# Performance work log

Hardware: AMD Instinct MI355X
Metric: run time of the kernel (lower is better)

## Reference

```python
import jax, jax.numpy as jnp
import numpy as np
import math

C = 128
LAM = 0.25
MARGIN = 0.3
TAU = math.log(C)
B = 8192


def lambertw(z, iters=10):
    """Principal-branch Lambert W via Halley iterations (valid for z >= -1/e)."""
    e = jnp.exp(1.0)
    # series init near the branch point z = -1/e, log init for z >= 0
    p = jnp.sqrt(jnp.maximum(2.0 * (e * z + 1.0), 0.0))
    w_near = -1.0 + p - p * p / 3.0 + (11.0 / 72.0) * p ** 3
    w = jnp.where(z < 0.0, w_near, jnp.log1p(jnp.maximum(z, 0.0)))
    for _ in range(iters):
        ew = jnp.exp(w)
        f = w * ew - z
        wp1 = w + 1.0
        w = w - f / (ew * wp1 - (w + 2.0) * f / (2.0 * wp1))
    return w


def triplet_loss(x, targets):
    # pairwise euclidean distances [B, B]
    sq = jnp.sum(x * x, axis=1)
    dist = sq[:, None] + sq[None, :] - 2.0 * (x @ x.T)
    dist = jnp.sqrt(jnp.maximum(dist, 1e-12))
    pos = targets[:, None] == targets[None, :]
    # hardest positive / hardest negative per anchor
    dist_ap = jnp.max(jnp.where(pos, dist, -jnp.inf), axis=1)
    dist_an = jnp.min(jnp.where(pos, jnp.inf, dist), axis=1)
    # MarginRankingLoss(margin)(dist_an, dist_ap, y=1), mean reduction
    return jnp.mean(jnp.maximum(dist_ap - dist_an + MARGIN, 0.0))


def cross_entropy(logits, targets):
    logp = jax.nn.log_softmax(logits, axis=-1)
    return -jnp.mean(jnp.take_along_axis(logp, targets[:, None], axis=1)[:, 0])


def setup_inputs() -> dict:
    key = jax.random.key(0)
    k1, k2 = jax.random.split(key)
    logits = jax.random.normal(k1, (B, C), dtype=jnp.float32)
    targets = jax.random.randint(k2, (B,), 0, C, dtype=jnp.int64)
    return {"logits": logits, "targets": targets}


def reference(logits, targets):
    # l_i is detached in the original (and sigma goes through numpy -> no grad)
    l_i = jax.lax.stop_gradient(triplet_loss(logits, targets))
    y = 0.5 * jnp.maximum(-2.0 / jnp.exp(1.0), (l_i - TAU) / LAM)
    sigma = jax.lax.stop_gradient(jnp.exp(-lambertw(y)))
    ce = cross_entropy(logits, targets)
    loss = (ce - TAU) * sigma + LAM * jnp.log(sigma) ** 2
    return jnp.sum(loss) / B
```

## Files before the change

kernel.cpp:

```cpp
#include <hip/hip_runtime.h>
#include <math.h>

#define NB 8192
#define NC 128
#define NJS 8
#define JPT 8

typedef float v4f __attribute__((ext_vector_type(4)));
typedef int   v8i __attribute__((ext_vector_type(8)));

__global__ __launch_bounds__(256) void k_prep(const float* __restrict__ x,
                                              const int* __restrict__ tgt,
                                              unsigned* __restrict__ xq,
                                              float* __restrict__ sq,
                                              float* __restrict__ ce,
                                              float* __restrict__ sums,
                                              unsigned* __restrict__ cnt) {
    int row = blockIdx.x * 8 + (threadIdx.x >> 5);
    int l = threadIdx.x & 31;
    float4 v = ((const float4*)(x + row * NC))[l];
    unsigned p = __builtin_amdgcn_cvt_pk_fp8_f32(v.x, v.y, 0, false);
    p = __builtin_amdgcn_cvt_pk_fp8_f32(v.z, v.w, p, true);
    xq[row * 32 + l] = p;

    float ss = fmaf(v.x, v.x, fmaf(v.y, v.y, fmaf(v.z, v.z, v.w * v.w)));
    float mx = fmaxf(fmaxf(v.x, v.y), fmaxf(v.z, v.w));
#pragma unroll
    for (int off = 16; off; off >>= 1) {
        ss += __shfl_xor(ss, off);
        mx = fmaxf(mx, __shfl_xor(mx, off));
    }
    float es = expf(v.x - mx) + expf(v.y - mx) + expf(v.z - mx) + expf(v.w - mx);
#pragma unroll
    for (int off = 16; off; off >>= 1) es += __shfl_xor(es, off);
    if (l == 0) {
        sq[row] = ss;
        ce[row] = mx + logf(es) - x[row * NC + tgt[row]];
    }
    if (blockIdx.x == 0 && threadIdx.x < 4) {
        if (threadIdx.x < 2) sums[threadIdx.x] = 0.0f;
        if (threadIdx.x == 2) *cnt = 0u;
    }
}

__global__ __launch_bounds__(256, 4) void k_trip(const unsigned char* __restrict__ xq,
                                                 const int* __restrict__ tgt,
                                                 const float* __restrict__ sq,
                                                 float* __restrict__ pmax,
                                                 float* __restrict__ pmin) {
    const int tid = threadIdx.x;
    const int lane = tid & 63;
    const int w = tid >> 6;
    const int rh = w >> 1;
    const int ch = w & 1;
    const int i0 = blockIdx.x * 64;
    const int jbase = blockIdx.y * 1024;
    const int m = lane & 15;
    const int quad = lane >> 4;

    v8i a[2];
#pragma unroll
    for (int tm = 0; tm < 2; ++tm) {
        int row = i0 + rh * 32 + tm * 16 + m;
        a[tm] = *(const v8i*)(xq + (size_t)row * 128 + quad * 32);
    }

    int ti[2][4];
#pragma unroll
    for (int tm = 0; tm < 2; ++tm)
#pragma unroll
        for (int r = 0; r < 4; ++r)
            ti[tm][r] = tgt[i0 + rh * 32 + tm * 16 + quad * 4 + r];

    float mp[2][4], mn[2][4];
#pragma unroll
    for (int tm = 0; tm < 2; ++tm)
#pragma unroll
        for (int r = 0; r < 4; ++r) { mp[tm][r] = -3.0e38f; mn[tm][r] = 3.0e38f; }

    const v4f z = {0.0f, 0.0f, 0.0f, 0.0f};

#pragma unroll
    for (int jt = 0; jt < JPT; ++jt) {
        int j0 = jbase + jt * 128;
#pragma unroll
        for (int tn = 0; tn < 4; ++tn) {
            int col = j0 + ch * 64 + tn * 16 + m;

            v8i b = *(const v8i*)(xq + (size_t)col * 128 + quad * 32);
            float sqj = sq[col];
            int tj = tgt[col];

            v4f acc0 = __builtin_amdgcn_mfma_scale_f32_16x16x128_f8f6f4(
                a[0], b, z, 0, 0, 0, 0x7f7f7f7f, 0, 0x7f7f7f7f);
            v4f acc1 = __builtin_amdgcn_mfma_scale_f32_16x16x128_f8f6f4(
                a[1], b, z, 0, 0, 0, 0x7f7f7f7f, 0, 0x7f7f7f7f);

#pragma unroll
            for (int r = 0; r < 4; ++r) {
                {
                    float v = fmaf(-2.0f, acc0[r], sqj);
                    bool pos = (tj == ti[0][r]);
                    mp[0][r] = fmaxf(mp[0][r], pos ? v : -3.0e38f);
                    mn[0][r] = fminf(mn[0][r], pos ? 3.0e38f : v);
                }
                {
                    float v = fmaf(-2.0f, acc1[r], sqj);
                    bool pos = (tj == ti[1][r]);
                    mp[1][r] = fmaxf(mp[1][r], pos ? v : -3.0e38f);
                    mn[1][r] = fminf(mn[1][r], pos ? 3.0e38f : v);
                }
            }
        }
    }

#pragma unroll
    for (int off = 1; off < 16; off <<= 1) {
#pragma unroll
        for (int tm = 0; tm < 2; ++tm)
#pragma unroll
            for (int r = 0; r < 4; ++r) {
                mp[tm][r] = fmaxf(mp[tm][r], __shfl_xor(mp[tm][r], off));
                mn[tm][r] = fminf(mn[tm][r], __shfl_xor(mn[tm][r], off));
            }
    }
    if (m == 0) {
        int slice = blockIdx.y * 2 + ch;
        float* pm = pmax + (size_t)slice * NB + i0 + rh * 32;
        float* pn = pmin + (size_t)slice * NB + i0 + rh * 32;
#pragma unroll
        for (int tm = 0; tm < 2; ++tm)
#pragma unroll
            for (int r = 0; r < 4; ++r) {
                int rr = tm * 16 + quad * 4 + r;
                pm[rr] = mp[tm][r];
                pn[rr] = mn[tm][r];
            }
    }
}

__global__ __launch_bounds__(256) void k_tail(const float* __restrict__ sq,
                                              const float* __restrict__ ce,
                                              const float* __restrict__ pmax,
                                              const float* __restrict__ pmin,
                                              float* __restrict__ sums,
                                              unsigned* __restrict__ cnt,
                                              float* __restrict__ out) {
    __shared__ float sh[4], sc[4];
    __shared__ unsigned lastFlag;
    const int tid = threadIdx.x;
    int i = blockIdx.x * 256 + tid;

    float vmax = -3.0e38f, vmin = 3.0e38f;
#pragma unroll
    for (int s = 0; s < 16; ++s) {
        vmax = fmaxf(vmax, pmax[s * NB + i]);
        vmin = fminf(vmin, pmin[s * NB + i]);
    }
    float sqi = sq[i];
    float ap = sqrtf(fmaxf(fmaxf(sqi + vmax, 0.0f), 1e-12f));
    float an = sqrtf(fmaxf(fmaxf(sqi + vmin, 0.0f), 1e-12f));
    float hs = fmaxf(ap - an + 0.3f, 0.0f);
    float cs = ce[i];
#pragma unroll
    for (int off = 32; off; off >>= 1) {
        hs += __shfl_xor(hs, off);
        cs += __shfl_xor(cs, off);
    }
    int wv = tid >> 6;
    if ((tid & 63) == 0) { sh[wv] = hs; sc[wv] = cs; }
    __syncthreads();
    if (tid == 0) {
        float H = sh[0] + sh[1] + sh[2] + sh[3];
        float Cs = sc[0] + sc[1] + sc[2] + sc[3];
        atomicAdd(sums + 0, H);
        atomicAdd(sums + 1, Cs);
        __threadfence();
        unsigned prev = atomicAdd(cnt, 1u);
        lastFlag = (prev == (unsigned)(gridDim.x - 1));
    }
    __syncthreads();
    if (!lastFlag || tid != 0) return;

    double H = (double)atomicAdd(sums + 0, 0.0f);
    double Cs = (double)atomicAdd(sums + 1, 0.0f);
    const double E = 2.71828182845904523536;
    const double TAU = log(128.0);
    const double LAMd = 0.25;
    double l = H / (double)NB;
    double cev = Cs / (double)NB;
    double y = 0.5 * fmax(-2.0 / E, (l - TAU) / LAMd);
    double p = sqrt(fmax(2.0 * (E * y + 1.0), 0.0));
    double wn = -1.0 + p - p * p / 3.0 + (11.0 / 72.0) * p * p * p;
    double wlw = (y < 0.0) ? wn : log1p(fmax(y, 0.0));
#pragma unroll
    for (int it = 0; it < 10; ++it) {
        double ew = exp(wlw);
        double f = wlw * ew - y;
        double wp1 = wlw + 1.0;
        wlw = wlw - f / (ew * wp1 - (wlw + 2.0) * f / (2.0 * wp1));
    }
    double sigma = exp(-wlw);
    double lg = log(sigma);
    double loss = (cev - TAU) * sigma + LAMd * lg * lg;
    out[0] = (float)(loss / (double)NB);
}

extern "C" void kernel_launch(void* const* d_in, const int* in_sizes, int n_in,
                              void* d_out, int out_size, void* d_ws, size_t ws_size,
                              hipStream_t stream) {
    const float* x = (const float*)d_in[0];
    const int* tgt = (const int*)d_in[1];
    float* out = (float*)d_out;

    unsigned char* xq = (unsigned char*)d_ws;
    float* sq = (float*)(xq + (size_t)NB * 128);
    float* ce = sq + NB;
    float* sums = ce + NB;
    unsigned* cnt = (unsigned*)(sums + 2);
    float* pmax = (float*)(cnt + 62);
    float* pmin = pmax + (size_t)16 * NB;

    k_prep<<<NB / 8, 256, 0, stream>>>(x, tgt, (unsigned*)xq, sq, ce, sums, cnt);
    dim3 grid(NB / 64, NJS);
    k_trip<<<grid, 256, 0, stream>>>(xq, tgt, sq, pmax, pmin);
    k_tail<<<NB / 256, 256, 0, stream>>>(sq, ce, pmax, pmin, sums, cnt, out);
}
```

Baseline: 100.5 us.

## Stage B tiles in LDS with double-buffered async loads, split column range further

The triplet kernel now copies each 128-column fp8 tile of the B operand into swizzled, double-buffered shared memory using global_load_lds. The next tile is prefetched while MFMAs run on the current one, replacing the scattered per-lane global loads. The grid doubles along the column dimension (16 slices of 512 columns, 32 partial slices), and the tail kernel is restructured so 8 thread groups reduce the 32 partials per row in parallel. This adds LDS use and barriers, which may limit occupancy, and doubles the partial-result traffic.

After: 112.1 us. +11.5%, slower.

```diff
diff --git a/kernel.cpp b/kernel.cpp
--- a/kernel.cpp
+++ b/kernel.cpp
@@ -3,8 +3,8 @@
 
 #define NB 8192
 #define NC 128
-#define NJS 8
-#define JPT 8
+#define NSL 16
+#define JPT 4
 
 typedef float v4f __attribute__((ext_vector_type(4)));
 typedef int   v8i __attribute__((ext_vector_type(8)));
@@ -43,20 +43,33 @@
     }
 }
 
-__global__ __launch_bounds__(256, 4) void k_trip(const unsigned char* __restrict__ xq,
+__global__ __launch_bounds__(256, 5) void k_trip(const unsigned char* __restrict__ xq,
                                                  const int* __restrict__ tgt,
                                                  const float* __restrict__ sq,
                                                  float* __restrict__ pmax,
                                                  float* __restrict__ pmin) {
+    __shared__ unsigned char Bs[2][128 * 128];
+
     const int tid = threadIdx.x;
     const int lane = tid & 63;
     const int w = tid >> 6;
     const int rh = w >> 1;
     const int ch = w & 1;
     const int i0 = blockIdx.x * 64;
-    const int jbase = blockIdx.y * 1024;
+    const int jbase = blockIdx.y * 512;
     const int m = lane & 15;
     const int quad = lane >> 4;
+
+#pragma unroll
+    for (int c = 0; c < 4; ++c) {
+        int L = w * 256 + c * 64 + lane;
+        int col = L >> 3, cc = L & 7;
+        const unsigned char* src = xq + (size_t)(jbase + col) * 128 + ((cc ^ (col & 7)) << 4);
+        __builtin_amdgcn_global_load_lds(
+            (const __attribute__((address_space(1))) unsigned*)src,
+            (__attribute__((address_space(3))) unsigned*)(&Bs[0][0] + (w * 256 + c * 64) * 16),
+            16, 0, 0);
+    }
 
     v8i a[2];
 #pragma unroll
@@ -78,18 +91,44 @@
 #pragma unroll
         for (int r = 0; r < 4; ++r) { mp[tm][r] = -3.0e38f; mn[tm][r] = 3.0e38f; }
 
-    const v4f z = {0.0f, 0.0f, 0.0f, 0.0f};
-
-#pragma unroll
+#pragma unroll 2
     for (int jt = 0; jt < JPT; ++jt) {
-        int j0 = jbase + jt * 128;
+        __syncthreads();
+
+        float sqj[4]; int tj[4];
 #pragma unroll
         for (int tn = 0; tn < 4; ++tn) {
-            int col = j0 + ch * 64 + tn * 16 + m;
-
-            v8i b = *(const v8i*)(xq + (size_t)col * 128 + quad * 32);
-            float sqj = sq[col];
-            int tj = tgt[col];
+            int col = jbase + jt * 128 + ch * 64 + tn * 16 + m;
+            sqj[tn] = sq[col];
+            tj[tn] = tgt[col];
+        }
+
+        if (jt + 1 < JPT) {
+            int jn = jbase + (jt + 1) * 128;
+            unsigned char* Bnxt = &Bs[(jt + 1) & 1][0];
+#pragma unroll
+            for (int c = 0; c < 4; ++c) {
+                int L = w * 256 + c * 64 + lane;
+                int col = L >> 3, cc = L & 7;
+                const unsigned char* src = xq + (size_t)(jn + col) * 128 + ((cc ^ (col & 7)) << 4);
+                __builtin_amdgcn_global_load_lds(
+                    (const __attribute__((address_space(1))) unsigned*)src,
+                    (__attribute__((address_space(3))) unsigned*)(Bnxt + (w * 256 + c * 64) * 16),
+                    16, 0, 0);
+            }
+        }
+
+        const unsigned char* Bcur = &Bs[jt & 1][0];
+        const v4f z = {0.0f, 0.0f, 0.0f, 0.0f};
+
+#pragma unroll
+        for (int tn = 0; tn < 4; ++tn) {
+            int cloc = ch * 64 + tn * 16 + m;
+
+            v8i b;
+            int base = cloc * 128;
+            *(int4*)&b = *(const int4*)(Bcur + base + ((((quad * 2) ^ (cloc & 7))) << 4));
+            *((int4*)&b + 1) = *(const int4*)(Bcur + base + ((((quad * 2 + 1) ^ (cloc & 7))) << 4));
 
             v4f acc0 = __builtin_amdgcn_mfma_scale_f32_16x16x128_f8f6f4(
                 a[0], b, z, 0, 0, 0, 0x7f7f7f7f, 0, 0x7f7f7f7f);
@@ -99,14 +138,14 @@
 #pragma unroll
             for (int r = 0; r < 4; ++r) {
                 {
-                    float v = fmaf(-2.0f, acc0[r], sqj);
-                    bool pos = (tj == ti[0][r]);
+                    float v = fmaf(-2.0f, acc0[r], sqj[tn]);
+                    bool pos = (tj[tn] == ti[0][r]);
                     mp[0][r] = fmaxf(mp[0][r], pos ? v : -3.0e38f);
                     mn[0][r] = fminf(mn[0][r], pos ? 3.0e38f : v);
                 }
                 {
-                    float v = fmaf(-2.0f, acc1[r], sqj);
-                    bool pos = (tj == ti[1][r]);
+                    float v = fmaf(-2.0f, acc1[r], sqj[tn]);
+                    bool pos = (tj[tn] == ti[1][r]);
                     mp[1][r] = fmaxf(mp[1][r], pos ? v : -3.0e38f);
                     mn[1][r] = fminf(mn[1][r], pos ? 3.0e38f : v);
                 }
@@ -146,35 +185,45 @@
                                               float* __restrict__ sums,
                                               unsigned* __restrict__ cnt,
                                               float* __restrict__ out) {
-    __shared__ float sh[4], sc[4];
+    __shared__ float smax[8][32], smin[8][32];
     __shared__ unsigned lastFlag;
     const int tid = threadIdx.x;
-    int i = blockIdx.x * 256 + tid;
+    const int a = tid & 31, g = tid >> 5;
+    const int i = blockIdx.x * 32 + a;
 
     float vmax = -3.0e38f, vmin = 3.0e38f;
 #pragma unroll
-    for (int s = 0; s < 16; ++s) {
-        vmax = fmaxf(vmax, pmax[s * NB + i]);
-        vmin = fminf(vmin, pmin[s * NB + i]);
-    }
-    float sqi = sq[i];
-    float ap = sqrtf(fmaxf(fmaxf(sqi + vmax, 0.0f), 1e-12f));
-    float an = sqrtf(fmaxf(fmaxf(sqi + vmin, 0.0f), 1e-12f));
-    float hs = fmaxf(ap - an + 0.3f, 0.0f);
-    float cs = ce[i];
-#pragma unroll
-    for (int off = 32; off; off >>= 1) {
+    for (int sl = g; sl < 32; sl += 8) {
+        vmax = fmaxf(vmax, pmax[(size_t)sl * NB + i]);
+        vmin = fminf(vmin, pmin[(size_t)sl * NB + i]);
+    }
+    smax[g][a] = vmax;
+    smin[g][a] = vmin;
+    __syncthreads();
+
+    float hs = 0.0f, cs = 0.0f;
+    if (tid < 32) {
+        float vx = smax[0][tid], vn = smin[0][tid];
+#pragma unroll
+        for (int k = 1; k < 8; ++k) {
+            vx = fmaxf(vx, smax[k][tid]);
+            vn = fminf(vn, smin[k][tid]);
+        }
+        int ii = blockIdx.x * 32 + tid;
+        float sqi = sq[ii];
+        float ap = sqrtf(fmaxf(fmaxf(sqi + vx, 0.0f), 1e-12f));
+        float an = sqrtf(fmaxf(fmaxf(sqi + vn, 0.0f), 1e-12f));
+        hs = fmaxf(ap - an + 0.3f, 0.0f);
+        cs = ce[ii];
+    }
+#pragma unroll
+    for (int off = 16; off; off >>= 1) {
         hs += __shfl_xor(hs, off);
         cs += __shfl_xor(cs, off);
     }
-    int wv = tid >> 6;
-    if ((tid & 63) == 0) { sh[wv] = hs; sc[wv] = cs; }
-    __syncthreads();
     if (tid == 0) {
-        float H = sh[0] + sh[1] + sh[2] + sh[3];
-        float Cs = sc[0] + sc[1] + sc[2] + sc[3];
-        atomicAdd(sums + 0, H);
-        atomicAdd(sums + 1, Cs);
+        atomicAdd(sums + 0, hs);
+        atomicAdd(sums + 1, cs);
         __threadfence();
         unsigned prev = atomicAdd(cnt, 1u);
         lastFlag = (prev == (unsigned)(gridDim.x - 1));
@@ -219,10 +268,10 @@
     float* sums = ce + NB;
     unsigned* cnt = (unsigned*)(sums + 2);
     float* pmax = (float*)(cnt + 62);
-    float* pmin = pmax + (size_t)16 * NB;
+    float* pmin = pmax + (size_t)32 * NB;
 
     k_prep<<<NB / 8, 256, 0, stream>>>(x, tgt, (unsigned*)xq, sq, ce, sums, cnt);
-    dim3 grid(NB / 64, NJS);
+    dim3 grid(NB / 64, NSL);
     k_trip<<<grid, 256, 0, stream>>>(xq, tgt, sq, pmax, pmin);
-    k_tail<<<NB / 256, 256, 0, stream>>>(sq, ce, pmax, pmin, sums, cnt, out);
-}
+    k_tail<<<NB / 32, 256, 0, stream>>>(sq, ce, pmax, pmin, sums, cnt, out);
+}
```
